# Performance work log

Hardware: AMD Instinct MI355X
Metric: run time of the kernel (lower is better)

## Reference

```python
import jax, jax.numpy as jnp
import numpy as np

HIDDEN = 1024

def setup_inputs() -> dict:
    key = jax.random.key(0)
    k1, k2, k3 = jax.random.split(key, 3)
    H = HIDDEN
    # xavier_uniform for [H, 4H] kernels: bound = sqrt(6/(H+4H))
    bound = float(np.sqrt(6.0 / (H + 4 * H)))
    x = jax.random.normal(k1, (32, 512, H), dtype=jnp.float32)
    input_kernel = jax.random.uniform(k2, (H, 4 * H), dtype=jnp.float32, minval=-bound, maxval=bound)
    hidden_kernel = jax.random.uniform(k3, (H, 4 * H), dtype=jnp.float32, minval=-bound, maxval=bound)
    bias = jnp.zeros((4 * H,), dtype=jnp.float32)
    return {"x": x, "input_kernel": input_kernel, "hidden_kernel": hidden_kernel, "bias": bias}

def _lstm(x, input_kernel, hidden_kernel, bias):
    B, S, H = x.shape
    # Precompute input projection for all timesteps as one big GEMM: [B,S,4H]
    xg = jnp.einsum('bsh,hg->bsg', x, input_kernel) + bias
    h0 = jnp.zeros((B, H), dtype=x.dtype)
    c0 = jnp.zeros((B, H), dtype=x.dtype)

    def step(carry, xg_t):
        h, c = carry
        gates = xg_t + h @ hidden_kernel  # [B, 4H]
        i_g, f_g, g_g, o_g = jnp.split(gates, 4, axis=-1)
        c = jax.nn.sigmoid(f_g) * c + jax.nn.sigmoid(i_g) * jnp.tanh(g_g)
        h = jax.nn.sigmoid(o_g) * jnp.tanh(c)
        return (h, c), h

    # scan over time axis: move S to leading dim
    (_, _), hs = jax.lax.scan(step, (h0, c0), jnp.swapaxes(xg, 0, 1))
    return jnp.swapaxes(hs, 0, 1)  # [B, S, H]

def reference(x, input_kernel, hidden_kernel, bias):
    return _lstm(x, input_kernel, hidden_kernel, bias)
```

## Files before the change

### kernel.cpp

```cpp
#include <hip/hip_runtime.h>


typedef __attribute__((ext_vector_type(4))) float f32x4_t;
typedef __attribute__((ext_vector_type(8))) short bf16x8_t;
typedef unsigned long long ull_t;

#define HID   1024
#define SLEN  512
#define NGATE 4096

#define XG_OFF    0ULL
#define RING_OFF  134217728ULL
#define WIT_OFF   167772160ULL
#define WHT_OFF   176160768ULL
#define FLAGS_OFF 184680448ULL
#define XB_OFF    RING_OFF

#define NBLK_B      256
#define FLAG_STRIDE 4
#define SLOT_SHORTS 32768

#define W_OFF_L   0
#define H_OFF_L   132096
#define G_OFF_L   148608
#define LDS_TOTAL 152768

__device__ __forceinline__ unsigned short f2bf(float f) {
  unsigned u = __float_as_uint(f);
  u += 0x7fffu + ((u >> 16) & 1u);
  return (unsigned short)(u >> 16);
}
__device__ __forceinline__ float bf2f(unsigned short u) {
  return __uint_as_float(((unsigned)u) << 16);
}
__device__ __forceinline__ float fast_rcp(float x) { return __builtin_amdgcn_rcpf(x); }
__device__ __forceinline__ float sigmoid_f(float x) { return fast_rcp(1.f + __expf(-x)); }
__device__ __forceinline__ float tanh_f(float x) { return 1.f - 2.f * fast_rcp(1.f + __expf(2.f * x)); }

__global__ __launch_bounds__(256) void conv_x_bf16(const float* __restrict__ in,
                                                   unsigned short* __restrict__ out) {
  size_t i = (size_t)blockIdx.x * 256 + threadIdx.x;
  const float4* p = (const float4*)in;
  float4 v = p[i];
  ushort4 o;
  o.x = f2bf(v.x); o.y = f2bf(v.y); o.z = f2bf(v.z); o.w = f2bf(v.w);
  ((ushort4*)out)[i] = o;
}

__global__ void transpose_w_bf16(const float* __restrict__ in,
                                 unsigned short* __restrict__ out) {
  __shared__ float tile[32][33];
  int tx = threadIdx.x, ty = threadIdx.y;
  int n0 = blockIdx.x * 32, k0 = blockIdx.y * 32;
  #pragma unroll
  for (int i = 0; i < 4; i++)
    tile[ty + 8 * i][tx] = in[(size_t)(k0 + ty + 8 * i) * NGATE + n0 + tx];
  __syncthreads();
  #pragma unroll
  for (int i = 0; i < 4; i++)
    out[(size_t)(n0 + ty + 8 * i) * HID + k0 + tx] = f2bf(tile[tx][ty + 8 * i]);
}

__global__ void init_ws(unsigned* __restrict__ flags) {
  int i = (int)blockIdx.x * 256 + threadIdx.x;
  if (i < NBLK_B * FLAG_STRIDE) flags[i] = 0u;
}

__global__ __launch_bounds__(256) void gemm_xg(const unsigned short* __restrict__ A,
                                               const unsigned short* __restrict__ BT,
                                               unsigned short* __restrict__ C) {
  extern __shared__ char smem[];
  char* As = smem;
  char* Bs = smem + 10240;
  const int tid = threadIdx.x;
  const int lane = tid & 63, w = tid >> 6, q = lane >> 4, l16 = lane & 15;
  const int wm = w & 1, wn = w >> 1;
  const size_t m0 = (size_t)blockIdx.y * 128, n0 = (size_t)blockIdx.x * 128;

  f32x4_t acc[4][4];
  #pragma unroll
  for (int i = 0; i < 4; i++)
    #pragma unroll
    for (int j = 0; j < 4; j++) acc[i][j] = (f32x4_t){0.f, 0.f, 0.f, 0.f};

  for (int kk = 0; kk < 32; kk++) {
    const int k0 = kk * 32;
    #pragma unroll
    for (int h = 0; h < 2; h++) {
      int idx = tid + h * 256;
      int r = idx >> 2, ch = idx & 3;
      uint4 va = *(const uint4*)((const char*)A + ((m0 + r) * HID + k0) * 2 + ch * 16);
      *(uint4*)(As + r * 80 + ch * 16) = va;
      uint4 vb = *(const uint4*)((const char*)BT + ((n0 + r) * HID + k0) * 2 + ch * 16);
      *(uint4*)(Bs + r * 80 + ch * 16) = vb;
    }
    __syncthreads();
    bf16x8_t af[4], bf[4];
    #pragma unroll
    for (int mt = 0; mt < 4; mt++)
      af[mt] = *(const bf16x8_t*)(As + (wm * 64 + mt * 16 + l16) * 80 + q * 16);
    #pragma unroll
    for (int nt = 0; nt < 4; nt++)
      bf[nt] = *(const bf16x8_t*)(Bs + (wn * 64 + nt * 16 + l16) * 80 + q * 16);
    #pragma unroll
    for (int mt = 0; mt < 4; mt++)
      #pragma unroll
      for (int nt = 0; nt < 4; nt++)
        acc[mt][nt] = __builtin_amdgcn_mfma_f32_16x16x32_bf16(af[mt], bf[nt], acc[mt][nt], 0, 0, 0);
    __syncthreads();
  }

  unsigned short* cst = (unsigned short*)smem;
  #pragma unroll
  for (int mt = 0; mt < 4; mt++)
    #pragma unroll
    for (int nt = 0; nt < 4; nt++)
      #pragma unroll
      for (int r = 0; r < 4; r++) {
        int m = wm * 64 + mt * 16 + q * 4 + r;
        int n = wn * 64 + nt * 16 + l16;
        cst[m * 136 + n] = f2bf(acc[mt][nt][r]);
      }
  __syncthreads();
  #pragma unroll
  for (int i = 0; i < 8; i++) {
    int idx = tid + i * 256;
    int row = idx >> 4, ch = idx & 15;
    uint4 v = *(const uint4*)((const char*)cst + row * 272 + ch * 16);
    *(uint4*)((char*)C + ((m0 + row) * NGATE + n0) * 2 + ch * 16) = v;
  }
}

__global__ __launch_bounds__(256) void lstm_persistent(
    const unsigned short* __restrict__ xg,
    const unsigned short* __restrict__ whT,
    const float* __restrict__ bias,
    float* __restrict__ out,
    unsigned short* ring,
    unsigned* flags) {
  extern __shared__ char smem[];
  char* w_lds = smem + W_OFF_L;
  char* h_lds = smem + H_OFF_L;
  float* gates = (float*)(smem + G_OFF_L);

  const int tid = threadIdx.x;
  const int lane = tid & 63, wv = tid >> 6, q = lane >> 4, l16 = lane & 15;
  const int g = blockIdx.x >> 6;
  const int m = blockIdx.x & 63;
  const int b_l = tid >> 4, j_l = tid & 15;

  for (int idx = tid; idx < 64 * 128; idx += 256) {
    int n = idx >> 7, ch = idx & 127;
    size_t gr = (size_t)(n >> 4) * 1024 + m * 16 + (n & 15);
    uint4 v = *(const uint4*)((const char*)whT + gr * 2048 + ch * 16);
    *(uint4*)(w_lds + n * 2064 + ch * 16) = v;
  }
  float bsr[4];
  #pragma unroll
  for (int G = 0; G < 4; G++) bsr[G] = bias[G * 1024 + m * 16 + j_l];
  float c_st = 0.f;
  const char* arow = h_lds + (l16 & 7) * 2064 + q * 16;
  const char* brow = w_lds + (wv * 16 + l16) * 2064 + q * 16;
  unsigned short* ring_g = ring + (size_t)g * 8192;
  unsigned* fl_g = flags + g * 64 * FLAG_STRIDE;
  __syncthreads();

  for (int t = 0; t < SLEN; t++) {
    unsigned short xgv[4];
    if (tid < 128) {
      const unsigned short* p =
          xg + ((size_t)(g * 8 + b_l) * 512 + t) * 4096 + m * 16 + j_l;
      xgv[0] = p[0]; xgv[1] = p[1024]; xgv[2] = p[2048]; xgv[3] = p[3072];
    }
    if (t > 0) {
      if (tid < 64) {
        const unsigned* fp = fl_g + tid * FLAG_STRIDE;
        while (__hip_atomic_load(fp, __ATOMIC_RELAXED, __HIP_MEMORY_SCOPE_AGENT) < (unsigned)t)
          __builtin_amdgcn_s_sleep(1);
      }
      __syncthreads();
      asm volatile("" ::: "memory");
      {
        const char* src = (const char*)(ring_g + (size_t)(t - 1) * SLOT_SHORTS);
        uint4 v0 = *(const uint4*)(src + tid * 16);
        uint4 v1 = *(const uint4*)(src + tid * 16 + 4096);
        uint4 v2 = *(const uint4*)(src + tid * 16 + 8192);
        uint4 v3 = *(const uint4*)(src + tid * 16 + 12288);
        int c0 = tid, c1 = tid + 256, c2 = tid + 512, c3 = tid + 768;
        *(uint4*)(h_lds + (c0 >> 7) * 2064 + (c0 & 127) * 16) = v0;
        *(uint4*)(h_lds + (c1 >> 7) * 2064 + (c1 & 127) * 16) = v1;
        *(uint4*)(h_lds + (c2 >> 7) * 2064 + (c2 & 127) * 16) = v2;
        *(uint4*)(h_lds + (c3 >> 7) * 2064 + (c3 & 127) * 16) = v3;
      }
    }
    __syncthreads();

    f32x4_t acc0 = (f32x4_t){0.f, 0.f, 0.f, 0.f};
    f32x4_t acc1 = (f32x4_t){0.f, 0.f, 0.f, 0.f};
    if (t > 0) {
      #pragma unroll
      for (int kk = 0; kk < 32; kk += 2) {
        bf16x8_t a0 = *(const bf16x8_t*)(arow + kk * 64);
        bf16x8_t b0 = *(const bf16x8_t*)(brow + kk * 64);
        acc0 = __builtin_amdgcn_mfma_f32_16x16x32_bf16(a0, b0, acc0, 0, 0, 0);
        bf16x8_t a1 = *(const bf16x8_t*)(arow + kk * 64 + 64);
        bf16x8_t b1 = *(const bf16x8_t*)(brow + kk * 64 + 64);
        acc1 = __builtin_amdgcn_mfma_f32_16x16x32_bf16(a1, b1, acc1, 0, 0, 0);
      }
    }
    #pragma unroll
    for (int r = 0; r < 4; r++) {
      int bb = q * 4 + r;
      gates[bb * 65 + wv * 16 + l16] = acc0[r] + acc1[r];
    }
    __syncthreads();

    if (tid < 128) {
      float gi = gates[b_l * 65 + j_l]      + bsr[0] + bf2f(xgv[0]);
      float gf = gates[b_l * 65 + 16 + j_l] + bsr[1] + bf2f(xgv[1]);
      float gg = gates[b_l * 65 + 32 + j_l] + bsr[2] + bf2f(xgv[2]);
      float go = gates[b_l * 65 + 48 + j_l] + bsr[3] + bf2f(xgv[3]);
      float i_s = sigmoid_f(gi), f_s = sigmoid_f(gf);
      float g_t = tanh_f(gg), o_s = sigmoid_f(go);
      c_st = f_s * c_st + i_s * g_t;
      float h = o_s * tanh_f(c_st);
      unsigned short hb = f2bf(h);
      unsigned other = __shfl_xor((unsigned)hb, 1);
      unsigned u = ((unsigned)hb & 0xffffu) | (other << 16);
      unsigned u2 = __shfl_xor(u, 2);
      if ((j_l & 3) == 0) {
        ull_t v8 = (ull_t)u | ((ull_t)u2 << 32);
        ull_t* dst = (ull_t*)(ring_g + (size_t)t * SLOT_SHORTS +
                              b_l * 1024 + m * 16 + j_l);
        __hip_atomic_store(dst, v8, __ATOMIC_RELAXED, __HIP_MEMORY_SCOPE_AGENT);
      }
      out[((size_t)(g * 8 + b_l) * 512 + t) * 1024 + m * 16 + j_l] = h;
    }
    asm volatile("s_waitcnt vmcnt(0)" ::: "memory");
    __syncthreads();
    if (tid == 0)
      __hip_atomic_store(fl_g + m * FLAG_STRIDE, (unsigned)(t + 1),
                         __ATOMIC_RELAXED, __HIP_MEMORY_SCOPE_AGENT);
  }
}

extern "C" void kernel_launch(void* const* d_in, const int* in_sizes, int n_in,
                              void* d_out, int out_size, void* d_ws, size_t ws_size,
                              hipStream_t stream) {
  const float* x    = (const float*)d_in[0];
  const float* wi   = (const float*)d_in[1];
  const float* wh   = (const float*)d_in[2];
  const float* bias = (const float*)d_in[3];
  float* out = (float*)d_out;

  char* ws = (char*)d_ws;
  unsigned short* xg   = (unsigned short*)(ws + XG_OFF);
  unsigned short* xb   = (unsigned short*)(ws + XB_OFF);
  unsigned short* ring = (unsigned short*)(ws + RING_OFF);
  unsigned short* wiT  = (unsigned short*)(ws + WIT_OFF);
  unsigned short* whT  = (unsigned short*)(ws + WHT_OFF);
  unsigned* flags      = (unsigned*)(ws + FLAGS_OFF);

  (void)hipFuncSetAttribute((const void*)lstm_persistent,
                            hipFuncAttributeMaxDynamicSharedMemorySize,
                            LDS_TOTAL);

  conv_x_bf16<<<16384, 256, 0, stream>>>(x, xb);
  transpose_w_bf16<<<dim3(128, 32), dim3(32, 8), 0, stream>>>(wi, wiT);
  transpose_w_bf16<<<dim3(128, 32), dim3(32, 8), 0, stream>>>(wh, whT);
  init_ws<<<4, 256, 0, stream>>>(flags);
  gemm_xg<<<dim3(32, 128), 256, 34816, stream>>>(xb, wiT, xg);
  lstm_persistent<<<NBLK_B, 256, LDS_TOTAL, stream>>>(xg, whT, bias, out, ring, flags);
}
```

Before: 2.197 ms.

## Hold recurrent weight fragments in registers instead of LDS in persistent LSTM

Each wave now loads its slice of the hidden-to-hidden weight matrix into 32 bf16x8 register fragments once, and feeds them straight into the MFMA loop. This replaces the per-step LDS reads of the weights and shrinks shared memory to the h and gates buffers only. The end-of-step wait now lets the output store stay in flight (vmcnt(1)) while the ring store must finish before the flag is published. The cost is much higher VGPR pressure (128 VGPRs of weights per thread), which carries a risk of spilling. The vmcnt ordering also relies on the ring store being issued before the out store.

```diff
diff --git a/kernel.cpp b/kernel.cpp
--- a/kernel.cpp
+++ b/kernel.cpp
@@ -19,11 +19,6 @@
 #define NBLK_B      256
 #define FLAG_STRIDE 4
 #define SLOT_SHORTS 32768
-
-#define W_OFF_L   0
-#define H_OFF_L   132096
-#define G_OFF_L   148608
-#define LDS_TOTAL 152768
 
 __device__ __forceinline__ unsigned short f2bf(float f) {
   unsigned u = __float_as_uint(f);
@@ -131,17 +126,15 @@
   }
 }
 
-__global__ __launch_bounds__(256) void lstm_persistent(
+__global__ __launch_bounds__(256, 1) void lstm_persistent(
     const unsigned short* __restrict__ xg,
     const unsigned short* __restrict__ whT,
     const float* __restrict__ bias,
     float* __restrict__ out,
     unsigned short* ring,
     unsigned* flags) {
-  extern __shared__ char smem[];
-  char* w_lds = smem + W_OFF_L;
-  char* h_lds = smem + H_OFF_L;
-  float* gates = (float*)(smem + G_OFF_L);
+  __shared__ __align__(16) char h_lds[8 * 2064];
+  __shared__ float gates[16 * 65];
 
   const int tid = threadIdx.x;
   const int lane = tid & 63, wv = tid >> 6, q = lane >> 4, l16 = lane & 15;
@@ -149,21 +142,24 @@
   const int m = blockIdx.x & 63;
   const int b_l = tid >> 4, j_l = tid & 15;
 
-  for (int idx = tid; idx < 64 * 128; idx += 256) {
-    int n = idx >> 7, ch = idx & 127;
-    size_t gr = (size_t)(n >> 4) * 1024 + m * 16 + (n & 15);
-    uint4 v = *(const uint4*)((const char*)whT + gr * 2048 + ch * 16);
-    *(uint4*)(w_lds + n * 2064 + ch * 16) = v;
+  bf16x8_t bfr[32];
+  {
+    const char* wrow = (const char*)whT +
+        ((size_t)(wv * 1024 + m * 16 + l16) * HID) * 2 + q * 16;
+    #pragma unroll
+    for (int kk = 0; kk < 32; kk++)
+      bfr[kk] = *(const bf16x8_t*)(wrow + kk * 64);
+    #pragma unroll
+    for (int kk = 0; kk < 32; kk++)
+      asm volatile("" : "+v"(bfr[kk]));
   }
   float bsr[4];
   #pragma unroll
   for (int G = 0; G < 4; G++) bsr[G] = bias[G * 1024 + m * 16 + j_l];
   float c_st = 0.f;
   const char* arow = h_lds + (l16 & 7) * 2064 + q * 16;
-  const char* brow = w_lds + (wv * 16 + l16) * 2064 + q * 16;
   unsigned short* ring_g = ring + (size_t)g * 8192;
   unsigned* fl_g = flags + g * 64 * FLAG_STRIDE;
-  __syncthreads();
 
   for (int t = 0; t < SLEN; t++) {
     unsigned short xgv[4];
@@ -201,11 +197,9 @@
       #pragma unroll
       for (int kk = 0; kk < 32; kk += 2) {
         bf16x8_t a0 = *(const bf16x8_t*)(arow + kk * 64);
-        bf16x8_t b0 = *(const bf16x8_t*)(brow + kk * 64);
-        acc0 = __builtin_amdgcn_mfma_f32_16x16x32_bf16(a0, b0, acc0, 0, 0, 0);
         bf16x8_t a1 = *(const bf16x8_t*)(arow + kk * 64 + 64);
-        bf16x8_t b1 = *(const bf16x8_t*)(brow + kk * 64 + 64);
-        acc1 = __builtin_amdgcn_mfma_f32_16x16x32_bf16(a1, b1, acc1, 0, 0, 0);
+        acc0 = __builtin_amdgcn_mfma_f32_16x16x32_bf16(a0, bfr[kk], acc0, 0, 0, 0);
+        acc1 = __builtin_amdgcn_mfma_f32_16x16x32_bf16(a1, bfr[kk + 1], acc1, 0, 0, 0);
       }
     }
     #pragma unroll
@@ -234,9 +228,10 @@
                               b_l * 1024 + m * 16 + j_l);
         __hip_atomic_store(dst, v8, __ATOMIC_RELAXED, __HIP_MEMORY_SCOPE_AGENT);
       }
+      asm volatile("" ::: "memory");
       out[((size_t)(g * 8 + b_l) * 512 + t) * 1024 + m * 16 + j_l] = h;
     }
-    asm volatile("s_waitcnt vmcnt(0)" ::: "memory");
+    asm volatile("s_waitcnt vmcnt(1)" ::: "memory");
     __syncthreads();
     if (tid == 0)
       __hip_atomic_store(fl_g + m * FLAG_STRIDE, (unsigned)(t + 1),
@@ -261,14 +256,10 @@
   unsigned short* whT  = (unsigned short*)(ws + WHT_OFF);
   unsigned* flags      = (unsigned*)(ws + FLAGS_OFF);
 
-  (void)hipFuncSetAttribute((const void*)lstm_persistent,
-                            hipFuncAttributeMaxDynamicSharedMemorySize,
-                            LDS_TOTAL);
-
   conv_x_bf16<<<16384, 256, 0, stream>>>(x, xb);
   transpose_w_bf16<<<dim3(128, 32), dim3(32, 8), 0, stream>>>(wi, wiT);
   transpose_w_bf16<<<dim3(128, 32), dim3(32, 8), 0, stream>>>(wh, whT);
   init_ws<<<4, 256, 0, stream>>>(flags);
   gemm_xg<<<dim3(32, 128), 256, 34816, stream>>>(xb, wiT, xg);
-  lstm_persistent<<<NBLK_B, 256, LDS_TOTAL, stream>>>(xg, whT, bias, out, ring, flags);
-}
+  lstm_persistent<<<NBLK_B, 256, 0, stream>>>(xg, whT, bias, out, ring, flags);
+}
```

Measured after the change: 1.930 ms. -12.1%, faster.
